# Kernel tuning notes

Hardware: AMD Instinct MI355X
Metric: run time of the kernel (lower is better)

The kernel has to match this reference:

```python
import jax, jax.numpy as jnp
import numpy as np

B, S, D, H = 2, 2048, 2048, 16
DH = D // H  # 128


def setup_inputs() -> dict:
    key = jax.random.key(0)
    ks = jax.random.split(key, 7)
    x = jax.random.normal(ks[0], (B, S, D), dtype=jnp.float32)
    # causal mask [b, s, s], True = attend
    mask = jnp.broadcast_to(jnp.tril(jnp.ones((S, S), dtype=bool)), (B, S, S))
    scale = 1.0 / np.sqrt(D)
    Wq = jax.random.normal(ks[1], (D, H, DH), dtype=jnp.float32) * scale
    Wk = jax.random.normal(ks[2], (D, 1, DH), dtype=jnp.float32) * scale
    Wv = jax.random.normal(ks[3], (D, 1, DH), dtype=jnp.float32) * scale
    Wo = jax.random.normal(ks[4], (H, DH, D), dtype=jnp.float32) * scale
    bo = jnp.zeros((D,), dtype=jnp.float32)
    return {"x": x, "mask": mask, "Wq": Wq, "Wk": Wk, "Wv": Wv, "Wo": Wo, "bo": bo}


def reference(x, mask, Wq, Wk, Wv, Wo, bo):
    # projections: q [b,s,h,dh]; k,v [b,s,1,dh] (single shared KV head)
    q = jnp.einsum("bsd,dhe->bshe", x, Wq)
    k = jnp.einsum("bsd,dhe->bshe", x, Wk)[:, :, 0, :]  # [b,s,dh]
    v = jnp.einsum("bsd,dhe->bshe", x, Wv)[:, :, 0, :]  # [b,s,dh]
    # scores [b,h,s,s] with 1/sqrt(d_head) scaling
    scores = jnp.einsum("bqhe,bke->bhqk", q, k) / jnp.sqrt(
        jnp.asarray(q.shape[-1], dtype=q.dtype)
    )
    big_neg = jnp.finfo(scores.dtype).min
    scores = jnp.where(mask[:, None, :, :], scores, big_neg)
    probs = jax.nn.softmax(scores, axis=-1)
    attn = jnp.einsum("bhqk,bke->bhqe", probs, v)  # [b,h,s,dh]
    # output projection contracting (head, d_head) -> d_state, with bias
    out = jnp.einsum("bhqe,hed->bqd", attn, Wo) + bo
    return out
```

## Files before the change

kernel.cpp:

```cpp
#include <hip/hip_runtime.h>
#include <cmath>
#include <cstdint>

typedef __bf16 bf16;
typedef __bf16 bf16x8 __attribute__((ext_vector_type(8)));
typedef __bf16 bf16x4 __attribute__((ext_vector_type(4)));
typedef float f32x4 __attribute__((ext_vector_type(4)));

#define SDIM 2048
#define DDIM 2048
#define NQKV 2304
#define DH   128

__device__ __forceinline__ void glds16(const bf16* g, bf16* l) {
    __builtin_amdgcn_global_load_lds(
        (const __attribute__((address_space(1))) void*)g,
        (__attribute__((address_space(3))) void*)l, 16, 0, 0);
}

#define MEMFENCE() asm volatile("" ::: "memory")
#define SBAR() do { MEMFENCE(); __builtin_amdgcn_s_barrier(); MEMFENCE(); } while (0)

__global__ __launch_bounds__(256) void prep_kernel(const float* __restrict__ x,
                                                   const float* __restrict__ Wq,
                                                   const float* __restrict__ Wk,
                                                   const float* __restrict__ Wv,
                                                   const float* __restrict__ Wo,
                                                   bf16* __restrict__ xb,
                                                   bf16* __restrict__ Wqkv_t,
                                                   bf16* __restrict__ Wo_t) {
    __shared__ float tile[32][33];
    int bx = blockIdx.x;
    if (bx < 8192) {
        int i = bx * 256 + threadIdx.x;
        float4 v = reinterpret_cast<const float4*>(x)[i];
        bf16x4 o;
        o[0] = (bf16)v.x; o[1] = (bf16)v.y; o[2] = (bf16)v.z; o[3] = (bf16)v.w;
        reinterpret_cast<bf16x4*>(xb)[i] = o;
        return;
    }
    bx -= 8192;
    const float* src; bf16* dst; int srcN; int t;
    if (bx < 4096)      { src = Wq; dst = Wqkv_t;                      srcN = 2048; t = bx; }
    else if (bx < 4352) { src = Wk; dst = Wqkv_t + (size_t)2048*2048;  srcN = 128;  t = bx - 4096; }
    else if (bx < 4608) { src = Wv; dst = Wqkv_t + (size_t)2176*2048;  srcN = 128;  t = bx - 4352; }
    else                { src = Wo; dst = Wo_t;                        srcN = 2048; t = bx - 4608; }
    const int srcK = 2048;
    int ntx = srcN >> 5;
    int n0 = (t % ntx) * 32, k0 = (t / ntx) * 32;
    int tx = threadIdx.x & 31;
    int ty = threadIdx.x >> 5;
    for (int i = 0; i < 4; i++)
        tile[ty + i*8][tx] = src[(size_t)(k0 + ty + i*8) * srcN + n0 + tx];
    __syncthreads();
    for (int i = 0; i < 4; i++)
        dst[(size_t)(n0 + ty + i*8) * srcK + k0 + tx] = (bf16)tile[tx][ty + i*8];
}

__global__ __launch_bounds__(256) void vtrans_kernel(const bf16* __restrict__ QKV,
                                                     bf16* __restrict__ Vt) {
    __shared__ bf16 tile[32][33];
    int tx = threadIdx.x & 31;
    int ty = threadIdx.x >> 5;
    int d0 = blockIdx.x * 32;
    int s0 = blockIdx.y * 32;
    int b  = blockIdx.z;
    for (int i = 0; i < 4; i++)
        tile[ty + i*8][tx] = QKV[((size_t)b * SDIM + s0 + ty + i*8) * NQKV + 2176 + d0 + tx];
    __syncthreads();
    int pos = s0 + tx;
    int pp = (pos & ~63) | (pos & 32) | ((pos & 12) << 1) | ((pos & 16) >> 2) | (pos & 3);
    for (int i = 0; i < 4; i++)
        Vt[((size_t)b * DH + d0 + ty + i*8) * SDIM + pp] = tile[tx][ty + i*8];
}

template<int WRITE_F32>
__global__ __launch_bounds__(512, 2) void gemm8_kernel(const bf16* __restrict__ A,
                                                       const bf16* __restrict__ Bt,
                                                       void* __restrict__ Cout,
                                                       const float* __restrict__ bias,
                                                       int N) {
    constexpr int K  = 2048;
    constexpr int NT = 32;
    __shared__ bf16 smem[65536];

    const int tid  = threadIdx.x;
    const int wave = tid >> 6, lane = tid & 63;
    const int quad = lane >> 4, l15 = lane & 15;
    const int wm = wave >> 2, wn = wave & 3;
    const int tm = blockIdx.x * 256, tn = blockIdx.y * 256;

    const int r0 = wave * 32 + (lane >> 2);
    const int cs = (lane & 3) ^ ((lane >> 3) & 3);
    const bf16* Ag = A  + (size_t)(tm + r0) * K + cs * 8;
    const bf16* Bg = Bt + (size_t)(tn + r0) * K + cs * 8;
    bf16* Asl = smem + wave * 1024;
    bf16* Bsl = smem + 32768 + wave * 1024;

    auto STAGE_A = [&](int t, int kh) {
        if (t < NT) {
            const bf16* s = Ag + t * 64 + kh * 32;
            bf16* d = Asl + (t & 1) * 16384 + kh * 8192;
            glds16(s, d);
            glds16(s + 16 * K, d + 512);
        }
    };
    auto STAGE_B = [&](int t, int kh) {
        if (t < NT) {
            const bf16* s = Bg + t * 64 + kh * 32;
            bf16* d = Bsl + (t & 1) * 16384 + kh * 8192;
            glds16(s, d);
            glds16(s + 16 * K, d + 512);
        }
    };

    const int rsw  = (l15 >> 1) & 3;
    const int aoff = (wm * 128 + l15) * 32 + ((quad ^ rsw) * 8);
    const int boff = (wn * 64  + l15) * 32 + ((quad ^ rsw) * 8);

    f32x4 acc[8][4];
#pragma unroll
    for (int m = 0; m < 8; m++)
#pragma unroll
        for (int n = 0; n < 4; n++) acc[m][n] = (f32x4)0.0f;

    STAGE_A(0, 0); STAGE_B(0, 0);
    STAGE_A(0, 1); STAGE_B(0, 1);
    STAGE_A(1, 0); STAGE_B(1, 0);
    asm volatile("s_waitcnt vmcnt(4)" ::: "memory");
    SBAR();

    bf16x8 av[4], bv[4];
    for (int t = 0; t < NT; ++t) {
        const int buf = t & 1;
        const bf16* Sa = smem + buf * 16384;
        const bf16* Sb = smem + 32768 + buf * 16384;

#pragma unroll
        for (int m = 0; m < 4; m++) av[m] = *reinterpret_cast<const bf16x8*>(Sa + aoff + m * 512);
#pragma unroll
        for (int n = 0; n < 4; n++) bv[n] = *reinterpret_cast<const bf16x8*>(Sb + boff + n * 512);
        STAGE_A(t + 1, 1);
        SBAR();
        __builtin_amdgcn_s_setprio(1);
#pragma unroll
        for (int m = 0; m < 4; m++)
#pragma unroll
            for (int n = 0; n < 4; n++)
                acc[m][n] = __builtin_amdgcn_mfma_f32_16x16x32_bf16(av[m], bv[n], acc[m][n], 0, 0, 0);
        __builtin_amdgcn_s_setprio(0);
        SBAR();

#pragma unroll
        for (int m = 0; m < 4; m++) av[m] = *reinterpret_cast<const bf16x8*>(Sa + aoff + 2048 + m * 512);
        STAGE_B(t + 1, 1);
        SBAR();
        __builtin_amdgcn_s_setprio(1);
#pragma unroll
        for (int m = 0; m < 4; m++)
#pragma unroll
            for (int n = 0; n < 4; n++)
                acc[4 + m][n] = __builtin_amdgcn_mfma_f32_16x16x32_bf16(av[m], bv[n], acc[4 + m][n], 0, 0, 0);
        __builtin_amdgcn_s_setprio(0);
        if (t + 1 < NT) { asm volatile("s_waitcnt vmcnt(8)" ::: "memory"); }
        else            { asm volatile("s_waitcnt vmcnt(0)" ::: "memory"); }
        SBAR();

#pragma unroll
        for (int m = 0; m < 4; m++) av[m] = *reinterpret_cast<const bf16x8*>(Sa + 8192 + aoff + m * 512);
#pragma unroll
        for (int n = 0; n < 4; n++) bv[n] = *reinterpret_cast<const bf16x8*>(Sb + 8192 + boff + n * 512);
        STAGE_A(t + 2, 0);
        SBAR();
        __builtin_amdgcn_s_setprio(1);
#pragma unroll
        for (int m = 0; m < 4; m++)
#pragma unroll
            for (int n = 0; n < 4; n++)
                acc[m][n] = __builtin_amdgcn_mfma_f32_16x16x32_bf16(av[m], bv[n], acc[m][n], 0, 0, 0);
        __builtin_amdgcn_s_setprio(0);
        SBAR();

#pragma unroll
        for (int m = 0; m < 4; m++) av[m] = *reinterpret_cast<const bf16x8*>(Sa + 8192 + aoff + 2048 + m * 512);
        STAGE_B(t + 2, 0);
        SBAR();
        __builtin_amdgcn_s_setprio(1);
#pragma unroll
        for (int m = 0; m < 4; m++)
#pragma unroll
            for (int n = 0; n < 4; n++)
                acc[4 + m][n] = __builtin_amdgcn_mfma_f32_16x16x32_bf16(av[m], bv[n], acc[4 + m][n], 0, 0, 0);
        __builtin_amdgcn_s_setprio(0);
        if (t + 2 < NT) { asm volatile("s_waitcnt vmcnt(4)" ::: "memory"); }
        else            { asm volatile("s_waitcnt vmcnt(0)" ::: "memory"); }
        SBAR();
    }

#pragma unroll
    for (int m = 0; m < 8; m++)
#pragma unroll
        for (int n = 0; n < 4; n++)
#pragma unroll
            for (int r = 0; r < 4; r++) {
                int row = tm + wm * 128 + m * 16 + quad * 4 + r;
                int col = tn + wn * 64 + n * 16 + l15;
                float v = acc[m][n][r];
                if (WRITE_F32)
                    reinterpret_cast<float*>(Cout)[(size_t)row * N + col] = v + bias[col];
                else
                    reinterpret_cast<bf16*>(Cout)[(size_t)row * N + col] = (bf16)v;
            }
}

__global__ __launch_bounds__(256) void flash_kernel(const bf16* __restrict__ QKV,
                                                    const bf16* __restrict__ Vt,
                                                    bf16* __restrict__ attn) {
    __shared__ __align__(16) bf16 KVS[32768];
    const int tid  = threadIdx.x;
    const int wave = tid >> 6, lane = tid & 63;
    const int quad = lane >> 4, l15 = lane & 15;
    const int bx = blockIdx.x;
    const int u  = (bx < 256) ? bx : bx - 256;
    const int qs = (bx < 256) ? (255 - (u >> 1)) : (u >> 1);
    const int b  = u & 1;
    const int q0 = qs * 8 + wave * 2;
    const size_t rowbase = (size_t)b * SDIM;
    const bf16* Vtb = Vt + (size_t)b * DH * SDIM;
    const float scale = 0.088388347648318447f;

    const bf16* kgp[4]; const bf16* vgp[4];
#pragma unroll
    for (int i = 0; i < 4; i++) {
        int s = wave * 4 + i;
        int krow = s * 4 + (lane >> 4);
        kgp[i] = QKV + (rowbase + krow) * NQKV + 2048 + (((lane & 15) ^ (krow & 15)) * 8);
        int vrow = s * 8 + (lane >> 3);
        vgp[i] = Vtb + (size_t)vrow * SDIM + (((lane & 7) ^ (vrow & 7)) * 8);
    }

    bf16x8 qf[2][4];
#pragma unroll
    for (int r2 = 0; r2 < 2; r2++) {
        const bf16* qp = QKV + (rowbase + q0 + r2) * NQKV + l15 * DH + quad * 8;
#pragma unroll
        for (int kk = 0; kk < 4; kk++) qf[r2][kk] = *reinterpret_cast<const bf16x8*>(qp + kk * 32);
    }

    f32x4 acc[2][8];
#pragma unroll
    for (int r2 = 0; r2 < 2; r2++)
#pragma unroll
        for (int d = 0; d < 8; d++) acc[r2][d] = (f32x4)0.0f;
    float l_s[2] = {0.0f, 0.0f};

    const int ntiles = (qs >> 3) + 1;

#pragma unroll
    for (int i = 0; i < 4; i++) {
        glds16(kgp[i], KVS + (wave*4 + i) * 512);
        glds16(vgp[i], KVS + 8192 + (wave*4 + i) * 512);
        kgp[i] += 64 * NQKV; vgp[i] += 64;
    }

    for (int t = 0; t < ntiles; t++) {
        if (t + 1 < ntiles) {
            const int bo = ((t + 1) & 1) << 14;
#pragma unroll
            for (int i = 0; i < 4; i++) {
                glds16(kgp[i], KVS + bo + (wave*4 + i) * 512);
                glds16(vgp[i], KVS + bo + 8192 + (wave*4 + i) * 512);
                kgp[i] += 64 * NQKV; vgp[i] += 64;
            }
            asm volatile("s_waitcnt vmcnt(8)" ::: "memory");
        } else {
            asm volatile("s_waitcnt vmcnt(0)" ::: "memory");
        }
        SBAR();
        const bf16* Ks  = KVS + ((t & 1) << 14);
        const bf16* Vts = Ks + 8192;
        const int key0 = t * 64;

        f32x4 sc[2][4];
#pragma unroll
        for (int r2 = 0; r2 < 2; r2++)
#pragma unroll
            for (int c = 0; c < 4; c++) sc[r2][c] = (f32x4)0.0f;
        __builtin_amdgcn_s_setprio(1);
#pragma unroll
        for (int c = 0; c < 4; c++)
#pragma unroll
            for (int kk = 0; kk < 4; kk++) {
                bf16x8 kf = *reinterpret_cast<const bf16x8*>(
                    Ks + (c*16 + l15) * 128 + (((kk*4 + quad) ^ l15) * 8));
                sc[0][c] = __builtin_amdgcn_mfma_f32_16x16x32_bf16(kf, qf[0][kk], sc[0][c], 0, 0, 0);
                sc[1][c] = __builtin_amdgcn_mfma_f32_16x16x32_bf16(kf, qf[1][kk], sc[1][c], 0, 0, 0);
            }
        __builtin_amdgcn_s_setprio(0);

        bf16x8 pa[2][2];
#pragma unroll
        for (int r2 = 0; r2 < 2; r2++) {
            const int q = q0 + r2;
            const bool tail = (key0 + 63 > q);
            float ps = 0.0f;
#pragma unroll
            for (int c = 0; c < 4; c++)
#pragma unroll
                for (int r = 0; r < 4; r++) {
                    int key = key0 + c*16 + quad*4 + r;
                    float pv = (tail && key > q) ? 0.0f : __expf(sc[r2][c][r] * scale);
                    ps += pv;
                    pa[r2][c >> 1][(c & 1)*4 + r] = (bf16)pv;
                }
            l_s[r2] += ps;
        }

        __builtin_amdgcn_s_setprio(1);
#pragma unroll
        for (int kk2 = 0; kk2 < 2; kk2++)
#pragma unroll
            for (int dd = 0; dd < 8; dd++) {
                bf16x8 vf = *reinterpret_cast<const bf16x8*>(
                    Vts + (dd*16 + l15) * 64 + (((kk2*4 + quad) ^ (l15 & 7)) * 8));
                acc[0][dd] = __builtin_amdgcn_mfma_f32_16x16x32_bf16(pa[0][kk2], vf, acc[0][dd], 0, 0, 0);
                acc[1][dd] = __builtin_amdgcn_mfma_f32_16x16x32_bf16(pa[1][kk2], vf, acc[1][dd], 0, 0, 0);
            }
        __builtin_amdgcn_s_setprio(0);
        SBAR();
    }

    __syncthreads();

    float linv[2];
#pragma unroll
    for (int r2 = 0; r2 < 2; r2++) {
        float v = l_s[r2];
        v += __shfl_xor(v, 16);
        v += __shfl_xor(v, 32);
        linv[r2] = 1.0f / v;
    }

    bf16* Ow = KVS + wave * 4096;
#pragma unroll
    for (int r2 = 0; r2 < 2; r2++)
#pragma unroll
        for (int r = 0; r < 4; r++) {
            float inv = __shfl(linv[r2], quad*4 + r);
#pragma unroll
            for (int dd = 0; dd < 8; dd++)
                Ow[r2*2048 + (quad*4 + r)*128 + dd*16 + l15] = (bf16)(acc[r2][dd][r] * inv);
        }
    __syncthreads();
    const int orow = lane >> 2;
    const int ocol = (lane & 3) * 8;
#pragma unroll
    for (int rr = 0; rr < 2; rr++) {
        bf16* ob = attn + (rowbase + q0 + rr) * (size_t)DDIM;
        const bf16* Os = KVS + wave * 4096 + rr * 2048;
#pragma unroll
        for (int it = 0; it < 4; it++)
            *reinterpret_cast<uint4*>(ob + orow * DH + ocol + it*32) =
                *reinterpret_cast<const uint4*>(Os + orow * 128 + ocol + it*32);
    }
}

extern "C" void kernel_launch(void* const* d_in, const int* in_sizes, int n_in,
                              void* d_out, int out_size, void* d_ws, size_t ws_size,
                              hipStream_t stream) {
    const float* x  = (const float*)d_in[0];
    const float* Wq = (const float*)d_in[2];
    const float* Wk = (const float*)d_in[3];
    const float* Wv = (const float*)d_in[4];
    const float* Wo = (const float*)d_in[5];
    const float* bo = (const float*)d_in[6];
    float* out = (float*)d_out;

    char* ws = (char*)d_ws;
    bf16* xb     = (bf16*)(ws);
    bf16* Wqkv_t = (bf16*)(ws + 16777216);
    bf16* Wo_t   = (bf16*)(ws + 26214400);
    bf16* QKV    = (bf16*)(ws + 34603008);
    bf16* attn   = (bf16*)(ws + 53477376);
    bf16* Vtb    = (bf16*)(ws + 70254592);
    (void)ws_size; (void)in_sizes; (void)n_in; (void)out_size;

    prep_kernel<<<16896, 256, 0, stream>>>(x, Wq, Wk, Wv, Wo, xb, Wqkv_t, Wo_t);
    gemm8_kernel<0><<<dim3(16, 9), 512, 0, stream>>>(xb, Wqkv_t, (void*)QKV, nullptr, 2304);
    vtrans_kernel<<<dim3(4, 64, 2), 256, 0, stream>>>(QKV, Vtb);
    flash_kernel<<<512, 256, 0, stream>>>(QKV, Vtb, attn);
    gemm8_kernel<1><<<dim3(16, 8), 512, 0, stream>>>(attn, Wo_t, (void*)out, bo, 2048);
}
```

Before: 307.9 us.

## Narrow output GEMM tile and split flash blocks to one query row per wave

The output-projection GEMM gets a template width parameter and uses 256x128 tiles, doubling its grid from 128 to 256 blocks so more CUs stay busy. The flash kernel moves to 512-thread blocks with 8 waves. Each wave now handles one query row instead of two, and the K/V tile loads are spread across more waves. This aims at better occupancy and latency hiding, at the cost of less K/V fragment reuse per wave and more LDS reads per MFMA.

```diff
diff --git a/kernel.cpp b/kernel.cpp
--- a/kernel.cpp
+++ b/kernel.cpp
@@ -74,7 +74,7 @@
         Vt[((size_t)b * DH + d0 + ty + i*8) * SDIM + pp] = tile[tx][ty + i*8];
 }
 
-template<int WRITE_F32>
+template<int WRITE_F32, int BNW>
 __global__ __launch_bounds__(512, 2) void gemm8_kernel(const bf16* __restrict__ A,
                                                        const bf16* __restrict__ Bt,
                                                        void* __restrict__ Cout,
@@ -82,20 +82,23 @@
                                                        int N) {
     constexpr int K  = 2048;
     constexpr int NT = 32;
-    __shared__ bf16 smem[65536];
+    constexpr int BN = 64 * BNW;
+    constexpr int BHALF = BN * 32;
+    __shared__ bf16 smem[32768 + 4 * BHALF];
 
     const int tid  = threadIdx.x;
     const int wave = tid >> 6, lane = tid & 63;
     const int quad = lane >> 4, l15 = lane & 15;
     const int wm = wave >> 2, wn = wave & 3;
-    const int tm = blockIdx.x * 256, tn = blockIdx.y * 256;
-
-    const int r0 = wave * 32 + (lane >> 2);
-    const int cs = (lane & 3) ^ ((lane >> 3) & 3);
-    const bf16* Ag = A  + (size_t)(tm + r0) * K + cs * 8;
-    const bf16* Bg = Bt + (size_t)(tn + r0) * K + cs * 8;
+    const int tm = blockIdx.x * 256, tn = blockIdx.y * BN;
+
+    const int r0  = wave * 32 + (lane >> 2);
+    const int r0b = (BNW == 4) ? r0 : (wave * 16 + (lane >> 2));
+    const int cs  = (lane & 3) ^ ((lane >> 3) & 3);
+    const bf16* Ag = A  + (size_t)(tm + r0)  * K + cs * 8;
+    const bf16* Bg = Bt + (size_t)(tn + r0b) * K + cs * 8;
     bf16* Asl = smem + wave * 1024;
-    bf16* Bsl = smem + 32768 + wave * 1024;
+    bf16* Bsl = smem + 32768 + wave * ((BNW == 4) ? 1024 : 512);
 
     auto STAGE_A = [&](int t, int kh) {
         if (t < NT) {
@@ -108,45 +111,46 @@
     auto STAGE_B = [&](int t, int kh) {
         if (t < NT) {
             const bf16* s = Bg + t * 64 + kh * 32;
-            bf16* d = Bsl + (t & 1) * 16384 + kh * 8192;
+            bf16* d = Bsl + (t & 1) * (2 * BHALF) + kh * BHALF;
             glds16(s, d);
-            glds16(s + 16 * K, d + 512);
+            if constexpr (BNW == 4) glds16(s + 16 * K, d + 512);
         }
     };
 
     const int rsw  = (l15 >> 1) & 3;
-    const int aoff = (wm * 128 + l15) * 32 + ((quad ^ rsw) * 8);
-    const int boff = (wn * 64  + l15) * 32 + ((quad ^ rsw) * 8);
-
-    f32x4 acc[8][4];
+    const int aoff = (wm * 128      + l15) * 32 + ((quad ^ rsw) * 8);
+    const int boff = (wn * 16 * BNW + l15) * 32 + ((quad ^ rsw) * 8);
+
+    f32x4 acc[8][BNW];
 #pragma unroll
     for (int m = 0; m < 8; m++)
 #pragma unroll
-        for (int n = 0; n < 4; n++) acc[m][n] = (f32x4)0.0f;
+        for (int n = 0; n < BNW; n++) acc[m][n] = (f32x4)0.0f;
 
     STAGE_A(0, 0); STAGE_B(0, 0);
     STAGE_A(0, 1); STAGE_B(0, 1);
     STAGE_A(1, 0); STAGE_B(1, 0);
-    asm volatile("s_waitcnt vmcnt(4)" ::: "memory");
+    if constexpr (BNW == 4) asm volatile("s_waitcnt vmcnt(4)" ::: "memory");
+    else                    asm volatile("s_waitcnt vmcnt(3)" ::: "memory");
     SBAR();
 
-    bf16x8 av[4], bv[4];
+    bf16x8 av[4], bv[BNW];
     for (int t = 0; t < NT; ++t) {
         const int buf = t & 1;
         const bf16* Sa = smem + buf * 16384;
-        const bf16* Sb = smem + 32768 + buf * 16384;
+        const bf16* Sb = smem + 32768 + buf * (2 * BHALF);
 
 #pragma unroll
         for (int m = 0; m < 4; m++) av[m] = *reinterpret_cast<const bf16x8*>(Sa + aoff + m * 512);
 #pragma unroll
-        for (int n = 0; n < 4; n++) bv[n] = *reinterpret_cast<const bf16x8*>(Sb + boff + n * 512);
+        for (int n = 0; n < BNW; n++) bv[n] = *reinterpret_cast<const bf16x8*>(Sb + boff + n * 512);
         STAGE_A(t + 1, 1);
         SBAR();
         __builtin_amdgcn_s_setprio(1);
 #pragma unroll
         for (int m = 0; m < 4; m++)
 #pragma unroll
-            for (int n = 0; n < 4; n++)
+            for (int n = 0; n < BNW; n++)
                 acc[m][n] = __builtin_amdgcn_mfma_f32_16x16x32_bf16(av[m], bv[n], acc[m][n], 0, 0, 0);
         __builtin_amdgcn_s_setprio(0);
         SBAR();
@@ -159,24 +163,28 @@
 #pragma unroll
         for (int m = 0; m < 4; m++)
 #pragma unroll
-            for (int n = 0; n < 4; n++)
+            for (int n = 0; n < BNW; n++)
                 acc[4 + m][n] = __builtin_amdgcn_mfma_f32_16x16x32_bf16(av[m], bv[n], acc[4 + m][n], 0, 0, 0);
         __builtin_amdgcn_s_setprio(0);
-        if (t + 1 < NT) { asm volatile("s_waitcnt vmcnt(8)" ::: "memory"); }
-        else            { asm volatile("s_waitcnt vmcnt(0)" ::: "memory"); }
+        if (t + 1 < NT) {
+            if constexpr (BNW == 4) asm volatile("s_waitcnt vmcnt(8)" ::: "memory");
+            else                    asm volatile("s_waitcnt vmcnt(6)" ::: "memory");
+        } else {
+            asm volatile("s_waitcnt vmcnt(0)" ::: "memory");
+        }
         SBAR();
 
 #pragma unroll
         for (int m = 0; m < 4; m++) av[m] = *reinterpret_cast<const bf16x8*>(Sa + 8192 + aoff + m * 512);
 #pragma unroll
-        for (int n = 0; n < 4; n++) bv[n] = *reinterpret_cast<const bf16x8*>(Sb + 8192 + boff + n * 512);
+        for (int n = 0; n < BNW; n++) bv[n] = *reinterpret_cast<const bf16x8*>(Sb + BHALF + boff + n * 512);
         STAGE_A(t + 2, 0);
         SBAR();
         __builtin_amdgcn_s_setprio(1);
 #pragma unroll
         for (int m = 0; m < 4; m++)
 #pragma unroll
-            for (int n = 0; n < 4; n++)
+            for (int n = 0; n < BNW; n++)
                 acc[m][n] = __builtin_amdgcn_mfma_f32_16x16x32_bf16(av[m], bv[n], acc[m][n], 0, 0, 0);
         __builtin_amdgcn_s_setprio(0);
         SBAR();
@@ -189,22 +197,26 @@
 #pragma unroll
         for (int m = 0; m < 4; m++)
 #pragma unroll
-            for (int n = 0; n < 4; n++)
+            for (int n = 0; n < BNW; n++)
                 acc[4 + m][n] = __builtin_amdgcn_mfma_f32_16x16x32_bf16(av[m], bv[n], acc[4 + m][n], 0, 0, 0);
         __builtin_amdgcn_s_setprio(0);
-        if (t + 2 < NT) { asm volatile("s_waitcnt vmcnt(4)" ::: "memory"); }
-        else            { asm volatile("s_waitcnt vmcnt(0)" ::: "memory"); }
+        if (t + 2 < NT) {
+            if constexpr (BNW == 4) asm volatile("s_waitcnt vmcnt(4)" ::: "memory");
+            else                    asm volatile("s_waitcnt vmcnt(3)" ::: "memory");
+        } else {
+            asm volatile("s_waitcnt vmcnt(0)" ::: "memory");
+        }
         SBAR();
     }
 
 #pragma unroll
     for (int m = 0; m < 8; m++)
 #pragma unroll
-        for (int n = 0; n < 4; n++)
+        for (int n = 0; n < BNW; n++)
 #pragma unroll
             for (int r = 0; r < 4; r++) {
                 int row = tm + wm * 128 + m * 16 + quad * 4 + r;
-                int col = tn + wn * 64 + n * 16 + l15;
+                int col = tn + wn * 16 * BNW + n * 16 + l15;
                 float v = acc[m][n][r];
                 if (WRITE_F32)
                     reinterpret_cast<float*>(Cout)[(size_t)row * N + col] = v + bias[col];
@@ -213,9 +225,9 @@
             }
 }
 
-__global__ __launch_bounds__(256) void flash_kernel(const bf16* __restrict__ QKV,
-                                                    const bf16* __restrict__ Vt,
-                                                    bf16* __restrict__ attn) {
+__global__ __launch_bounds__(512, 4) void flash_kernel(const bf16* __restrict__ QKV,
+                                                       const bf16* __restrict__ Vt,
+                                                       bf16* __restrict__ attn) {
     __shared__ __align__(16) bf16 KVS[32768];
     const int tid  = threadIdx.x;
     const int wave = tid >> 6, lane = tid & 63;
@@ -224,55 +236,44 @@
     const int u  = (bx < 256) ? bx : bx - 256;
     const int qs = (bx < 256) ? (255 - (u >> 1)) : (u >> 1);
     const int b  = u & 1;
-    const int q0 = qs * 8 + wave * 2;
+    const int q  = qs * 8 + wave;
     const size_t rowbase = (size_t)b * SDIM;
     const bf16* Vtb = Vt + (size_t)b * DH * SDIM;
     const float scale = 0.088388347648318447f;
 
-    const bf16* kgp[4]; const bf16* vgp[4];
-#pragma unroll
-    for (int i = 0; i < 4; i++) {
-        int s = wave * 4 + i;
-        int krow = s * 4 + (lane >> 4);
-        kgp[i] = QKV + (rowbase + krow) * NQKV + 2048 + (((lane & 15) ^ (krow & 15)) * 8);
-        int vrow = s * 8 + (lane >> 3);
-        vgp[i] = Vtb + (size_t)vrow * SDIM + (((lane & 7) ^ (vrow & 7)) * 8);
-    }
-
-    bf16x8 qf[2][4];
-#pragma unroll
-    for (int r2 = 0; r2 < 2; r2++) {
-        const bf16* qp = QKV + (rowbase + q0 + r2) * NQKV + l15 * DH + quad * 8;
-#pragma unroll
-        for (int kk = 0; kk < 4; kk++) qf[r2][kk] = *reinterpret_cast<const bf16x8*>(qp + kk * 32);
-    }
-
-    f32x4 acc[2][8];
-#pragma unroll
-    for (int r2 = 0; r2 < 2; r2++)
-#pragma unroll
-        for (int d = 0; d < 8; d++) acc[r2][d] = (f32x4)0.0f;
-    float l_s[2] = {0.0f, 0.0f};
+    const int s0 = wave, s1 = wave + 8;
+    const int krow0 = s0*4 + quad, krow1 = s1*4 + quad;
+    const bf16* kp0 = QKV + (rowbase + krow0) * NQKV + 2048 + ((l15 ^ (krow0 & 15)) * 8);
+    const bf16* kp1 = QKV + (rowbase + krow1) * NQKV + 2048 + ((l15 ^ (krow1 & 15)) * 8);
+    const int vrow0 = s0*8 + (lane >> 3), vrow1 = s1*8 + (lane >> 3);
+    const bf16* vp0 = Vtb + (size_t)vrow0 * SDIM + (((lane & 7) ^ (vrow0 & 7)) * 8);
+    const bf16* vp1 = Vtb + (size_t)vrow1 * SDIM + (((lane & 7) ^ (vrow1 & 7)) * 8);
+
+    bf16x8 qf[4];
+    {
+        const bf16* qp = QKV + (rowbase + q) * NQKV + l15 * DH + quad * 8;
+#pragma unroll
+        for (int kk = 0; kk < 4; kk++) qf[kk] = *reinterpret_cast<const bf16x8*>(qp + kk * 32);
+    }
+
+    f32x4 acc[8];
+#pragma unroll
+    for (int d = 0; d < 8; d++) acc[d] = (f32x4)0.0f;
+    float l_s = 0.0f;
 
     const int ntiles = (qs >> 3) + 1;
 
-#pragma unroll
-    for (int i = 0; i < 4; i++) {
-        glds16(kgp[i], KVS + (wave*4 + i) * 512);
-        glds16(vgp[i], KVS + 8192 + (wave*4 + i) * 512);
-        kgp[i] += 64 * NQKV; vgp[i] += 64;
-    }
+    glds16(kp0, KVS + s0 * 512);        glds16(kp1, KVS + s1 * 512);
+    glds16(vp0, KVS + 8192 + s0 * 512); glds16(vp1, KVS + 8192 + s1 * 512);
+    kp0 += 64 * NQKV; kp1 += 64 * NQKV; vp0 += 64; vp1 += 64;
 
     for (int t = 0; t < ntiles; t++) {
         if (t + 1 < ntiles) {
             const int bo = ((t + 1) & 1) << 14;
-#pragma unroll
-            for (int i = 0; i < 4; i++) {
-                glds16(kgp[i], KVS + bo + (wave*4 + i) * 512);
-                glds16(vgp[i], KVS + bo + 8192 + (wave*4 + i) * 512);
-                kgp[i] += 64 * NQKV; vgp[i] += 64;
-            }
-            asm volatile("s_waitcnt vmcnt(8)" ::: "memory");
+            glds16(kp0, KVS + bo + s0 * 512);        glds16(kp1, KVS + bo + s1 * 512);
+            glds16(vp0, KVS + bo + 8192 + s0 * 512); glds16(vp1, KVS + bo + 8192 + s1 * 512);
+            kp0 += 64 * NQKV; kp1 += 64 * NQKV; vp0 += 64; vp1 += 64;
+            asm volatile("s_waitcnt vmcnt(4)" ::: "memory");
         } else {
             asm volatile("s_waitcnt vmcnt(0)" ::: "memory");
         }
@@ -281,11 +282,9 @@
         const bf16* Vts = Ks + 8192;
         const int key0 = t * 64;
 
-        f32x4 sc[2][4];
-#pragma unroll
-        for (int r2 = 0; r2 < 2; r2++)
-#pragma unroll
-            for (int c = 0; c < 4; c++) sc[r2][c] = (f32x4)0.0f;
+        f32x4 sc[4];
+#pragma unroll
+        for (int c = 0; c < 4; c++) sc[c] = (f32x4)0.0f;
         __builtin_amdgcn_s_setprio(1);
 #pragma unroll
         for (int c = 0; c < 4; c++)
@@ -293,15 +292,12 @@
             for (int kk = 0; kk < 4; kk++) {
                 bf16x8 kf = *reinterpret_cast<const bf16x8*>(
                     Ks + (c*16 + l15) * 128 + (((kk*4 + quad) ^ l15) * 8));
-                sc[0][c] = __builtin_amdgcn_mfma_f32_16x16x32_bf16(kf, qf[0][kk], sc[0][c], 0, 0, 0);
-                sc[1][c] = __builtin_amdgcn_mfma_f32_16x16x32_bf16(kf, qf[1][kk], sc[1][c], 0, 0, 0);
+                sc[c] = __builtin_amdgcn_mfma_f32_16x16x32_bf16(kf, qf[kk], sc[c], 0, 0, 0);
             }
         __builtin_amdgcn_s_setprio(0);
 
-        bf16x8 pa[2][2];
-#pragma unroll
-        for (int r2 = 0; r2 < 2; r2++) {
-            const int q = q0 + r2;
+        bf16x8 pa[2];
+        {
             const bool tail = (key0 + 63 > q);
             float ps = 0.0f;
 #pragma unroll
@@ -309,11 +305,11 @@
 #pragma unroll
                 for (int r = 0; r < 4; r++) {
                     int key = key0 + c*16 + quad*4 + r;
-                    float pv = (tail && key > q) ? 0.0f : __expf(sc[r2][c][r] * scale);
+                    float pv = (tail && key > q) ? 0.0f : __expf(sc[c][r] * scale);
                     ps += pv;
-                    pa[r2][c >> 1][(c & 1)*4 + r] = (bf16)pv;
+                    pa[c >> 1][(c & 1)*4 + r] = (bf16)pv;
                 }
-            l_s[r2] += ps;
+            l_s += ps;
         }
 
         __builtin_amdgcn_s_setprio(1);
@@ -323,8 +319,7 @@
             for (int dd = 0; dd < 8; dd++) {
                 bf16x8 vf = *reinterpret_cast<const bf16x8*>(
                     Vts + (dd*16 + l15) * 64 + (((kk2*4 + quad) ^ (l15 & 7)) * 8));
-                acc[0][dd] = __builtin_amdgcn_mfma_f32_16x16x32_bf16(pa[0][kk2], vf, acc[0][dd], 0, 0, 0);
-                acc[1][dd] = __builtin_amdgcn_mfma_f32_16x16x32_bf16(pa[1][kk2], vf, acc[1][dd], 0, 0, 0);
+                acc[dd] = __builtin_amdgcn_mfma_f32_16x16x32_bf16(pa[kk2], vf, acc[dd], 0, 0, 0);
             }
         __builtin_amdgcn_s_setprio(0);
         SBAR();
@@ -332,37 +327,29 @@
 
     __syncthreads();
 
-    float linv[2];
-#pragma unroll
-    for (int r2 = 0; r2 < 2; r2++) {
-        float v = l_s[r2];
+    float linv;
+    {
+        float v = l_s;
         v += __shfl_xor(v, 16);
         v += __shfl_xor(v, 32);
-        linv[r2] = 1.0f / v;
-    }
-
-    bf16* Ow = KVS + wave * 4096;
-#pragma unroll
-    for (int r2 = 0; r2 < 2; r2++)
-#pragma unroll
-        for (int r = 0; r < 4; r++) {
-            float inv = __shfl(linv[r2], quad*4 + r);
-#pragma unroll
-            for (int dd = 0; dd < 8; dd++)
-                Ow[r2*2048 + (quad*4 + r)*128 + dd*16 + l15] = (bf16)(acc[r2][dd][r] * inv);
-        }
-    __syncthreads();
+        linv = 1.0f / v;
+    }
+
+    bf16* Ow = KVS + wave * 2048;
+#pragma unroll
+    for (int r = 0; r < 4; r++) {
+        float inv = __shfl(linv, quad*4 + r);
+#pragma unroll
+        for (int dd = 0; dd < 8; dd++)
+            Ow[(quad*4 + r)*128 + dd*16 + l15] = (bf16)(acc[dd][r] * inv);
+    }
     const int orow = lane >> 2;
     const int ocol = (lane & 3) * 8;
-#pragma unroll
-    for (int rr = 0; rr < 2; rr++) {
-        bf16* ob = attn + (rowbase + q0 + rr) * (size_t)DDIM;
-        const bf16* Os = KVS + wave * 4096 + rr * 2048;
-#pragma unroll
-        for (int it = 0; it < 4; it++)
-            *reinterpret_cast<uint4*>(ob + orow * DH + ocol + it*32) =
-                *reinterpret_cast<const uint4*>(Os + orow * 128 + ocol + it*32);
-    }
+    bf16* ob = attn + (rowbase + q) * (size_t)DDIM;
+#pragma unroll
+    for (int it = 0; it < 4; it++)
+        *reinterpret_cast<uint4*>(ob + orow * DH + ocol + it*32) =
+            *reinterpret_cast<const uint4*>(Ow + orow * 128 + ocol + it*32);
 }
 
 extern "C" void kernel_launch(void* const* d_in, const int* in_sizes, int n_in,
@@ -386,8 +373,8 @@
     (void)ws_size; (void)in_sizes; (void)n_in; (void)out_size;
 
     prep_kernel<<<16896, 256, 0, stream>>>(x, Wq, Wk, Wv, Wo, xb, Wqkv_t, Wo_t);
-    gemm8_kernel<0><<<dim3(16, 9), 512, 0, stream>>>(xb, Wqkv_t, (void*)QKV, nullptr, 2304);
+    gemm8_kernel<0, 4><<<dim3(16, 9), 512, 0, stream>>>(xb, Wqkv_t, (void*)QKV, nullptr, 2304);
     vtrans_kernel<<<dim3(4, 64, 2), 256, 0, stream>>>(QKV, Vtb);
-    flash_kernel<<<512, 256, 0, stream>>>(QKV, Vtb, attn);
-    gemm8_kernel<1><<<dim3(16, 8), 512, 0, stream>>>(attn, Wo_t, (void*)out, bo, 2048);
-}
+    flash_kernel<<<512, 512, 0, stream>>>(QKV, Vtb, attn);
+    gemm8_kernel<1, 2><<<dim3(16, 16), 512, 0, stream>>>(attn, Wo_t, (void*)out, bo, 2048);
+}
```

Result: faster. 285.5 us (-7.3%).
